# Kernel optimization log

Hardware: AMD Instinct MI355X
Metric: run time of the kernel (lower is better)

The kernel has to match this reference:

```python
import jax, jax.numpy as jnp
import numpy as np
from jax import lax

D_MODEL, D_INNER, D_STATE, D_CONV, DT_RANK = 128, 256, 16, 4, 8
BATCH, SEQ = 8, 4096


def setup_inputs() -> dict:
    key = jax.random.key(0)
    ks = jax.random.split(key, 13)
    g = lambda k, shape, fan: (jax.random.normal(k, shape, jnp.float32) / np.sqrt(fan)).astype(jnp.float32)
    inp = {
        "s": jax.random.normal(ks[0], (BATCH, SEQ, D_MODEL), jnp.float32),
        "in_proj_w": g(ks[1], (2 * D_INNER, D_MODEL), D_MODEL),
        "conv_w": g(ks[2], (D_INNER, 1, D_CONV), D_CONV),
        "conv_b": jnp.zeros((D_INNER,), jnp.float32),
        "x_proj_w": g(ks[3], (DT_RANK + 2 * D_STATE, D_INNER), D_INNER),
        "dt_proj_w": g(ks[4], (D_INNER, DT_RANK), DT_RANK),
        "dt_proj_b": jax.random.uniform(ks[5], (D_INNER,), jnp.float32, -4.0, -2.0),  # softplus(b) small, like mamba dt init
        "A_log": jnp.log(jnp.broadcast_to(jnp.arange(1, D_STATE + 1, dtype=jnp.float32), (D_INNER, D_STATE))),
        "D_skip": jnp.ones((D_INNER,), jnp.float32),
        "out_proj_w": g(ks[6], (D_MODEL, D_INNER), D_INNER),
        "ln_gamma": jnp.ones((D_MODEL,), jnp.float32),
        "ln_beta": jnp.zeros((D_MODEL,), jnp.float32),
        "fc_w": g(ks[7], (D_MODEL, D_MODEL), D_MODEL),
    }
    return inp


def _mamba(s, in_proj_w, conv_w, conv_b, x_proj_w, dt_proj_w, dt_proj_b, A_log, D_skip, out_proj_w):
    B, L, _ = s.shape
    xz = jnp.einsum("bld,ed->ble", s, in_proj_w)           # [B,L,2*D_INNER]
    x, z = jnp.split(xz, 2, axis=-1)                        # each [B,L,D_INNER]
    # causal depthwise conv1d
    xc = jnp.transpose(x, (0, 2, 1))                        # [B,D_INNER,L]
    xc = jnp.pad(xc, ((0, 0), (0, 0), (D_CONV - 1, 0)))
    xc = lax.conv_general_dilated(xc, conv_w, (1,), "VALID",
                                  dimension_numbers=("NCH", "OIH", "NCH"),
                                  feature_group_count=D_INNER)
    x = jax.nn.silu(jnp.transpose(xc + conv_b[None, :, None], (0, 2, 1)))  # [B,L,D_INNER]
    # input-dependent dt, B, C
    x_dbl = jnp.einsum("bld,ed->ble", x, x_proj_w)
    dt = x_dbl[..., :DT_RANK]
    Bc = x_dbl[..., DT_RANK:DT_RANK + D_STATE]              # [B,L,D_STATE]
    Cc = x_dbl[..., DT_RANK + D_STATE:]                     # [B,L,D_STATE]
    dt = jax.nn.softplus(jnp.einsum("blr,dr->bld", dt, dt_proj_w) + dt_proj_b)  # [B,L,D_INNER]
    A = -jnp.exp(A_log)                                     # [D_INNER,D_STATE]

    def step(h, inp):
        dt_t, b_t, c_t, u_t = inp                           # [B,Di],[B,Ds],[B,Ds],[B,Di]
        dA = jnp.exp(dt_t[:, :, None] * A)                  # [B,Di,Ds]
        dBu = (dt_t * u_t)[:, :, None] * b_t[:, None, :]
        h = dA * h + dBu
        y = jnp.einsum("bds,bs->bd", h, c_t)
        return h, y

    h0 = jnp.zeros((B, D_INNER, D_STATE), x.dtype)
    xs = (jnp.swapaxes(dt, 0, 1), jnp.swapaxes(Bc, 0, 1), jnp.swapaxes(Cc, 0, 1), jnp.swapaxes(x, 0, 1))
    _, ys = lax.scan(step, h0, xs)                          # ys: [L,B,D_INNER]
    y = jnp.swapaxes(ys, 0, 1) + x * D_skip
    y = y * jax.nn.silu(z)
    return jnp.einsum("bld,od->blo", y, out_proj_w)         # [B,L,D_MODEL]


def reference(s, in_proj_w, conv_w, conv_b, x_proj_w, dt_proj_w, dt_proj_b, A_log, D_skip, out_proj_w, ln_gamma, ln_beta, fc_w):
    h = _mamba(s, in_proj_w, conv_w, conv_b, x_proj_w, dt_proj_w, dt_proj_b, A_log, D_skip, out_proj_w)
    mu = jnp.mean(h, axis=-1, keepdims=True)
    var = jnp.mean(jnp.square(h - mu), axis=-1, keepdims=True)
    hn = (h - mu) * lax.rsqrt(var + 1e-5) * ln_gamma + ln_beta
    return jax.nn.relu(jnp.einsum("bld,od->blo", hn, fc_w))
```

## Files before the change

kernel.cpp:

```cpp
#include <hip/hip_runtime.h>
#include <math.h>

#define B_ 8
#define L_ 4096
#define DM 128
#define DI 256
#define DSN 16
#define RK 8
#define M_ (B_*L_)
#define NC 128
#define CH 32
#define CH2 64

typedef __attribute__((ext_vector_type(8))) short bfrag;
typedef __attribute__((ext_vector_type(4))) float ffrag;
typedef __attribute__((ext_vector_type(2))) float f32x2;

__device__ __forceinline__ float silu_f(float x) {
  return x * __builtin_amdgcn_rcpf(1.f + __expf(-x));
}
__device__ __forceinline__ float softplus_f(float x) {
  return (x > 20.f) ? x : __logf(1.f + __expf(x));
}

__device__ __forceinline__ unsigned short f2bf(float f) {
  unsigned int u = __builtin_bit_cast(unsigned int, f);
  unsigned int r = (u + 0x7FFFu + ((u >> 16) & 1u)) >> 16;
  return (unsigned short)r;
}
__device__ __forceinline__ unsigned int f2bf2(float lo, float hi) {
  return (unsigned int)f2bf(lo) | ((unsigned int)f2bf(hi) << 16);
}
__device__ __forceinline__ float bf2f(unsigned int us) {
  return __builtin_bit_cast(float, us << 16);
}

__global__ __launch_bounds__(256)
void gemm_bf16_in(const float* __restrict__ A, const float* __restrict__ W,
                  unsigned short* __restrict__ xb, unsigned short* __restrict__ zsb) {
  __shared__ unsigned short As[64 * 136];
  __shared__ unsigned short Ws[64 * 136];
  __shared__ unsigned short Os[64 * 72];
  const int t = threadIdx.x;
  const int m0 = blockIdx.y << 6;
  const int half = blockIdx.x;
  unsigned short* __restrict__ outp = half ? zsb : xb;
  const float* __restrict__ Wbase = W + (half << 8) * 128;
  for (int i = t; i < 64 * 32; i += 256) {
    int row = i >> 5, c4 = i & 31;
    float4 av = *(const float4*)&A[(m0 + row) * 128 + (c4 << 2)];
    uint2 ap = {f2bf2(av.x, av.y), f2bf2(av.z, av.w)};
    *(uint2*)&As[row * 136 + (c4 << 2)] = ap;
  }
  float4 wr[8];
#pragma unroll
  for (int k = 0; k < 8; ++k) {
    int i = t + (k << 8);
    int row = i >> 5, c4 = i & 31;
    wr[k] = *(const float4*)&Wbase[row * 128 + (c4 << 2)];
  }
#pragma unroll
  for (int k = 0; k < 8; ++k) {
    int i = t + (k << 8);
    int row = i >> 5, c4 = i & 31;
    uint2 wp = {f2bf2(wr[k].x, wr[k].y), f2bf2(wr[k].z, wr[k].w)};
    *(uint2*)&Ws[row * 136 + (c4 << 2)] = wp;
  }
  __syncthreads();
  const int w = t >> 6, l = t & 63, q = l >> 4, col = l & 15;
  for (int jt = 0; jt < 4; ++jt) {
    if (jt < 3) {
#pragma unroll
      for (int k = 0; k < 8; ++k) {
        int i = t + (k << 8);
        int row = i >> 5, c4 = i & 31;
        wr[k] = *(const float4*)&Wbase[(((jt + 1) << 6) + row) * 128 + (c4 << 2)];
      }
    }
    ffrag acc[4] = {{0.f,0.f,0.f,0.f},{0.f,0.f,0.f,0.f},{0.f,0.f,0.f,0.f},{0.f,0.f,0.f,0.f}};
#pragma unroll
    for (int s = 0; s < 4; ++s) {
      int k0 = s * 32 + q * 8;
      bfrag af = *(const bfrag*)&As[((w << 4) + col) * 136 + k0];
#pragma unroll
      for (int nt = 0; nt < 4; ++nt) {
        bfrag bf_ = *(const bfrag*)&Ws[((nt << 4) + col) * 136 + k0];
        acc[nt] = __builtin_amdgcn_mfma_f32_16x16x32_bf16(af, bf_, acc[nt], 0, 0, 0);
      }
    }
    __syncthreads();
#pragma unroll
    for (int nt = 0; nt < 4; ++nt)
#pragma unroll
      for (int i = 0; i < 4; ++i) {
        int ml = (w << 4) + (q << 2) + i;
        float v = acc[nt][i];
        if (half) v = silu_f(v);
        Os[ml * 72 + (nt << 4) + col] = f2bf(v);
      }
    if (jt < 3) {
#pragma unroll
      for (int k = 0; k < 8; ++k) {
        int i = t + (k << 8);
        int row = i >> 5, c4 = i & 31;
        uint2 wp = {f2bf2(wr[k].x, wr[k].y), f2bf2(wr[k].z, wr[k].w)};
        *(uint2*)&Ws[row * 136 + (c4 << 2)] = wp;
      }
    }
    __syncthreads();
    {
      int r = t >> 2, c8 = (t & 3) << 3;
      int m = m0 + r;
      *(uint4*)&outp[m * 256 + (jt << 6) + c8]      = *(const uint4*)&Os[r * 72 + c8];
      *(uint4*)&outp[m * 256 + (jt << 6) + 32 + c8] = *(const uint4*)&Os[r * 72 + 32 + c8];
    }
  }
}

__global__ __launch_bounds__(512)
void xproj_dtproj(const unsigned short* __restrict__ xb, const float* __restrict__ xw,
                  const float* __restrict__ dtw, const float* __restrict__ dtpb,
                  const float* __restrict__ cw, const float* __restrict__ cb,
                  const float* __restrict__ alog,
                  float* __restrict__ Bb, float* __restrict__ Cb,
                  unsigned int* __restrict__ udt,
                  unsigned short* __restrict__ cP, unsigned short* __restrict__ cHe) {
  __shared__ unsigned short ua[64 * 264];
  __shared__ unsigned short wb[48 * 264];
  __shared__ float dtr_s[64 * 12];
  __shared__ float Bs_l[64 * 16];
  const int t = threadIdx.x;
  const int p0 = blockIdx.x << 6;
  {
    const int k = t & 255, half = t >> 8;
    const int pstart = half << 5;
    const int base = p0 + pstart;
    const int lb = base & (L_ - 1);
    const float w0 = cw[k*4], w1 = cw[k*4+1], w2 = cw[k*4+2], w3 = cw[k*4+3];
    const float bias = cb[k];
    float x0 = (lb >= 3) ? bf2f((unsigned int)xb[(base - 3) * 256 + k]) : 0.f;
    float x1 = (lb >= 2) ? bf2f((unsigned int)xb[(base - 2) * 256 + k]) : 0.f;
    float x2 = (lb >= 1) ? bf2f((unsigned int)xb[(base - 1) * 256 + k]) : 0.f;
#pragma unroll 8
    for (int it = 0; it < 32; ++it) {
      float x3 = bf2f((unsigned int)xb[(base + it) * 256 + k]);
      float u = silu_f(fmaf(w0, x0, fmaf(w1, x1, fmaf(w2, x2, fmaf(w3, x3, bias)))));
      ua[(pstart + it) * 264 + k] = f2bf(u);
      x0 = x1; x1 = x2; x2 = x3;
    }
  }
  for (int i = t; i < 40 * 256; i += 512) {
    int n = i >> 8, k = i & 255;
    wb[n * 264 + k] = f2bf(xw[i]);
  }
  for (int i = t; i < 8 * 264; i += 512) wb[40 * 264 + i] = 0;
  __syncthreads();
  const int w = t >> 6, l = t & 63, q = l >> 4, col = l & 15;
  for (int tile = w; tile < 12; tile += 8) {
    const int mt = tile & 3, nt = tile >> 2;
    ffrag acc = {0.f, 0.f, 0.f, 0.f};
#pragma unroll
    for (int s = 0; s < 8; ++s) {
      int k0 = s * 32 + q * 8;
      bfrag af = *(const bfrag*)&ua[((mt << 4) + col) * 264 + k0];
      bfrag bf_ = *(const bfrag*)&wb[((nt << 4) + col) * 264 + k0];
      acc = __builtin_amdgcn_mfma_f32_16x16x32_bf16(af, bf_, acc, 0, 0, 0);
    }
#pragma unroll
    for (int i = 0; i < 4; ++i) {
      int ml = (mt << 4) + (q << 2) + i;
      int m = p0 + ml;
      if (nt == 0) {
        if (col < 8) dtr_s[ml * 12 + col] = acc[i];
        else {
          Bb[m * 16 + (col - 8)] = acc[i];
          Bs_l[ml * 16 + (col - 8)] = acc[i];
        }
      } else if (nt == 1) {
        if (col < 8) {
          Bb[m * 16 + 8 + col] = acc[i];
          Bs_l[ml * 16 + 8 + col] = acc[i];
        } else {
          Cb[m * 16 + (col - 8)] = acc[i];
        }
      } else {
        if (col < 8) Cb[m * 16 + 8 + col] = acc[i];
      }
    }
  }
  __syncthreads();
  {
    const int d = t & 255, half = t >> 8;
    const int pstart = half << 5;
    const int gpos = p0 + pstart;
    const int bb = gpos >> 12;
    const int cc = (gpos & (L_ - 1)) >> 5;
    const int bc = bb * NC + cc;
    float w8[8];
    *(float4*)&w8[0] = *(const float4*)&dtw[d * 8];
    *(float4*)&w8[4] = *(const float4*)&dtw[d * 8 + 4];
    const float bias = dtpb[d];
    float a[16];
    bool okl = true;
#pragma unroll
    for (int j = 0; j < 16; ++j) {
      a[j] = -__expf(alog[d * 16 + j]);
      float tgt = (float)(j + 1);
      okl = okl && (fabsf(a[j] + tgt) <= 1e-3f * tgt);
    }
    const bool fast = (bool)__all((int)okl);
    f32x2 h2[8] = {{0.f,0.f},{0.f,0.f},{0.f,0.f},{0.f,0.f},
                   {0.f,0.f},{0.f,0.f},{0.f,0.f},{0.f,0.f}};
    float sdt = 0.f;
#pragma unroll 2
    for (int pp = pstart; pp < pstart + 32; ++pp) {
      float r0[8];
      *(float4*)&r0[0] = *(const float4*)&dtr_s[pp * 12];
      *(float4*)&r0[4] = *(const float4*)&dtr_s[pp * 12 + 4];
      float a2 = bias;
#pragma unroll
      for (int r2 = 0; r2 < 8; ++r2) a2 = fmaf(r0[r2], w8[r2], a2);
      float sp = softplus_f(a2);
      unsigned int uq = (unsigned int)ua[pp * 264 + d];
      unsigned short spb = f2bf(sp);
      udt[(p0 + pp) * 256 + d] = uq | ((unsigned int)spb << 16);
      float dtv = bf2f((unsigned int)spb);
      float uv  = bf2f(uq);
      float du = dtv * uv;
      sdt += dtv;
      const float* brow = &Bs_l[pp * 16];
      float4 b0 = *(const float4*)&brow[0];
      float4 b1 = *(const float4*)&brow[4];
      float4 b2 = *(const float4*)&brow[8];
      float4 b3 = *(const float4*)&brow[12];
      f32x2 B2[8] = {{b0.x,b0.y},{b0.z,b0.w},{b1.x,b1.y},{b1.z,b1.w},
                     {b2.x,b2.y},{b2.z,b2.w},{b3.x,b3.y},{b3.z,b3.w}};
      f32x2 du2 = {du, du};
      if (fast) {
        float e1 = __expf(-dtv);
        float e2 = e1 * e1;
        f32x2 dA = {e1, e2};
        f32x2 e22 = {e2, e2};
#pragma unroll
        for (int jj = 0; jj < 8; ++jj) {
          h2[jj] = dA * h2[jj] + du2 * B2[jj];
          dA = dA * e22;
        }
      } else {
#pragma unroll
        for (int j = 0; j < 16; ++j) {
          float dA = __expf(dtv * a[j]);
          h2[j >> 1][j & 1] = fmaf(dA, h2[j >> 1][j & 1], du * B2[j >> 1][j & 1]);
        }
      }
    }
#pragma unroll
    for (int j = 0; j < 16; ++j) {
      int o = (bc * 16 + j) * 256 + d;
      cP[o]  = f2bf(__expf(a[j] * sdt));
      cHe[o] = f2bf(h2[j >> 1][j & 1]);
    }
  }
}

__global__ __launch_bounds__(512)
void scan_combine(unsigned short* __restrict__ cP, const unsigned short* __restrict__ cHe) {
  __shared__ float segP[64 * 9], segH[64 * 9], segS[64 * 9];
  const int t = threadIdx.x;
  const int sdl = t & 63, seg = t >> 6;
  const int blk = blockIdx.x;
  const int b = blk >> 6, grp = blk & 63;
  const int sd = (grp << 6) + sdl;
  const int base = b * NC * 4096 + sd;
  float Pacc = 1.f, Hacc = 0.f;
#pragma unroll
  for (int i = 0; i < 16; ++i) {
    int idx = base + (seg * 16 + i) * 4096;
    float p = bf2f((unsigned int)cP[idx]);
    float he = bf2f((unsigned int)cHe[idx]);
    Hacc = fmaf(p, Hacc, he);
    Pacc *= p;
  }
  segP[sdl * 9 + seg] = Pacc;
  segH[sdl * 9 + seg] = Hacc;
  __syncthreads();
  if (t < 64) {
    float hs = 0.f;
#pragma unroll
    for (int s2 = 0; s2 < 8; ++s2) {
      segS[t * 9 + s2] = hs;
      hs = fmaf(segP[t * 9 + s2], hs, segH[t * 9 + s2]);
    }
  }
  __syncthreads();
  float hs = segS[sdl * 9 + seg];
#pragma unroll
  for (int i = 0; i < 16; ++i) {
    int idx = base + (seg * 16 + i) * 4096;
    float p = bf2f((unsigned int)cP[idx]);
    float he = bf2f((unsigned int)cHe[idx]);
    cP[idx] = f2bf(hs);
    hs = fmaf(p, hs, he);
  }
}

__global__ __launch_bounds__(512, 4)
void scan3_out_ln_fc(const unsigned int* __restrict__ udt,
                     const float* __restrict__ Bb, const float* __restrict__ Cb,
                     const float* __restrict__ alog, const unsigned short* __restrict__ hst,
                     const float* __restrict__ dsk,
                     const unsigned short* __restrict__ zsb,
                     const float* __restrict__ W,
                     const float* __restrict__ gamma, const float* __restrict__ beta,
                     const float* __restrict__ fcw, float* __restrict__ out) {
  __shared__ float Bs[CH2 * 16];
  __shared__ float Cs[CH2 * 16];
  __shared__ unsigned short smA[64 * 264];
  __shared__ unsigned short smB[128 * 136];
  const int bc = blockIdx.x;
  const int b = bc >> 6, cc = bc & 63;
  const int t = threadIdx.x;
  const int l = t & 63, w = t >> 6;
  const int chh = t >> 8;
  const int d = t & 255;
  const int base = b * L_ + (cc << 1) * CH;
  const int cbase = base + chh * CH;
  const int hc = b * NC + (cc << 1) + chh;
  if (t < CH2 * 4)           ((float4*)Bs)[t]            = *(const float4*)&Bb[base * 16 + (t << 2)];
  else if (t < CH2 * 8)      ((float4*)Cs)[t - CH2 * 4]  = *(const float4*)&Cb[base * 16 + ((t - CH2 * 4) << 2)];
  float a[16];
  bool okl = true;
#pragma unroll
  for (int j = 0; j < 16; ++j) {
    a[j] = -__expf(alog[d * 16 + j]);
    float tgt = (float)(j + 1);
    okl = okl && (fabsf(a[j] + tgt) <= 1e-3f * tgt);
  }
  const bool fast = (bool)__all((int)okl);
  const float dskv = dsk[d];
  f32x2 h2[8];
#pragma unroll
  for (int jj = 0; jj < 8; ++jj) {
    h2[jj][0] = bf2f((unsigned int)hst[(hc * 16 + (jj << 1)) * 256 + d]);
    h2[jj][1] = bf2f((unsigned int)hst[(hc * 16 + (jj << 1) + 1) * 256 + d]);
  }
  unsigned int wv0 = udt[cbase * 256 + d];
  unsigned int wv1 = udt[(cbase + 1) * 256 + d];
  unsigned short zv0 = zsb[cbase * 256 + d];
  unsigned short zv1 = zsb[(cbase + 1) * 256 + d];
  __syncthreads();
#pragma unroll 2
  for (int ll = 0; ll < CH; ++ll) {
    const int l2 = (ll + 2 < CH) ? ll + 2 : CH - 1;
    unsigned int wv2 = udt[(cbase + l2) * 256 + d];
    unsigned short zv2 = zsb[(cbase + l2) * 256 + d];
    const float* brow = &Bs[(chh * CH + ll) * 16];
    const float* crow = &Cs[(chh * CH + ll) * 16];
    float4 b0 = *(const float4*)&brow[0];
    float4 b1 = *(const float4*)&brow[4];
    float4 b2 = *(const float4*)&brow[8];
    float4 b3 = *(const float4*)&brow[12];
    float4 c0 = *(const float4*)&crow[0];
    float4 c1 = *(const float4*)&crow[4];
    float4 c2 = *(const float4*)&crow[8];
    float4 c3 = *(const float4*)&crow[12];
    float uv  = bf2f(wv0 & 0xFFFFu);
    float dtv = bf2f(wv0 >> 16);
    f32x2 B2[8] = {{b0.x,b0.y},{b0.z,b0.w},{b1.x,b1.y},{b1.z,b1.w},
                   {b2.x,b2.y},{b2.z,b2.w},{b3.x,b3.y},{b3.z,b3.w}};
    f32x2 C2[8] = {{c0.x,c0.y},{c0.z,c0.w},{c1.x,c1.y},{c1.z,c1.w},
                   {c2.x,c2.y},{c2.z,c2.w},{c3.x,c3.y},{c3.z,c3.w}};
    float du = dtv * uv;
    f32x2 du2 = {du, du};
    f32x2 y2 = {0.f, 0.f};
    if (fast) {
      float e1 = __expf(-dtv);
      float e2 = e1 * e1;
      f32x2 dA = {e1, e2};
      f32x2 e22 = {e2, e2};
#pragma unroll
      for (int jj = 0; jj < 8; ++jj) {
        h2[jj] = dA * h2[jj] + du2 * B2[jj];
        y2 = y2 + h2[jj] * C2[jj];
        dA = dA * e22;
      }
    } else {
#pragma unroll
      for (int j = 0; j < 16; ++j) {
        float dA = __expf(dtv * a[j]);
        float hh = fmaf(dA, h2[j >> 1][j & 1], du * B2[j >> 1][j & 1]);
        h2[j >> 1][j & 1] = hh;
        y2[j & 1] = fmaf(hh, C2[j >> 1][j & 1], y2[j & 1]);
      }
    }
    float y = y2.x + y2.y;
    float zs = bf2f((unsigned int)zv0);
    smA[(chh * CH + ll) * 264 + d] = f2bf(fmaf(uv, dskv, y) * zs);
    wv0 = wv1; wv1 = wv2; zv0 = zv1; zv1 = zv2;
  }
  const int q = l >> 4, col = l & 15;
  ffrag acc[2][4];
  for (int nt2 = 0; nt2 < 2; ++nt2) {
    __syncthreads();
    for (int i = t; i < 64 * 64; i += 512) {
      int row = i >> 6, c4 = i & 63;
      float4 wv = *(const float4*)&W[((nt2 << 6) + row) * 256 + (c4 << 2)];
      uint2 wp = {f2bf2(wv.x, wv.y), f2bf2(wv.z, wv.w)};
      *(uint2*)&smB[row * 264 + (c4 << 2)] = wp;
    }
    __syncthreads();
    if (t < 256) {
#pragma unroll
      for (int nt = 0; nt < 4; ++nt) acc[nt2][nt] = (ffrag){0.f, 0.f, 0.f, 0.f};
#pragma unroll
      for (int s = 0; s < 8; ++s) {
        int k0 = s * 32 + q * 8;
        bfrag af = *(const bfrag*)&smA[((w << 4) + col) * 264 + k0];
#pragma unroll
        for (int nt = 0; nt < 4; ++nt) {
          bfrag bf_ = *(const bfrag*)&smB[((nt << 4) + col) * 264 + k0];
          acc[nt2][nt] = __builtin_amdgcn_mfma_f32_16x16x32_bf16(af, bf_, acc[nt2][nt], 0, 0, 0);
        }
      }
    }
  }
  float mu[4], rs[4];
  if (t < 256) {
#pragma unroll
    for (int i = 0; i < 4; ++i) {
      float s1 = 0.f, s2 = 0.f;
#pragma unroll
      for (int nt2 = 0; nt2 < 2; ++nt2)
#pragma unroll
        for (int nt = 0; nt < 4; ++nt) {
          float v = acc[nt2][nt][i];
          s1 += v; s2 = fmaf(v, v, s2);
        }
      s1 += __shfl_xor(s1, 1); s2 += __shfl_xor(s2, 1);
      s1 += __shfl_xor(s1, 2); s2 += __shfl_xor(s2, 2);
      s1 += __shfl_xor(s1, 4); s2 += __shfl_xor(s2, 4);
      s1 += __shfl_xor(s1, 8); s2 += __shfl_xor(s2, 8);
      mu[i] = s1 * (1.f / DM);
      float var = s2 * (1.f / DM) - mu[i] * mu[i];
      rs[i] = rsqrtf(var + 1e-5f);
    }
  }
  __syncthreads();
  if (t < 256) {
#pragma unroll
    for (int nt2 = 0; nt2 < 2; ++nt2)
#pragma unroll
      for (int nt = 0; nt < 4; ++nt) {
        int n = (nt2 << 6) + (nt << 4) + col;
        float g = gamma[n], be = beta[n];
#pragma unroll
        for (int i = 0; i < 4; ++i) {
          int r = (w << 4) + (q << 2) + i;
          smA[r * 136 + n] = f2bf(fmaf((acc[nt2][nt][i] - mu[i]) * rs[i], g, be));
        }
      }
  }
  for (int i = t; i < 128 * 32; i += 512) {
    int row = i >> 5, c4 = i & 31;
    float4 wv = *(const float4*)&fcw[row * 128 + (c4 << 2)];
    uint2 wp = {f2bf2(wv.x, wv.y), f2bf2(wv.z, wv.w)};
    *(uint2*)&smB[row * 136 + (c4 << 2)] = wp;
  }
  __syncthreads();
  if (t < 256) {
    ffrag a2[8] = {{0.f,0.f,0.f,0.f},{0.f,0.f,0.f,0.f},{0.f,0.f,0.f,0.f},{0.f,0.f,0.f,0.f},
                   {0.f,0.f,0.f,0.f},{0.f,0.f,0.f,0.f},{0.f,0.f,0.f,0.f},{0.f,0.f,0.f,0.f}};
#pragma unroll
    for (int s = 0; s < 4; ++s) {
      int k0 = s * 32 + q * 8;
      bfrag af = *(const bfrag*)&smA[((w << 4) + col) * 136 + k0];
#pragma unroll
      for (int nt = 0; nt < 8; ++nt) {
        bfrag bf_ = *(const bfrag*)&smB[((nt << 4) + col) * 136 + k0];
        a2[nt] = __builtin_amdgcn_mfma_f32_16x16x32_bf16(af, bf_, a2[nt], 0, 0, 0);
      }
    }
#pragma unroll
    for (int nt = 0; nt < 8; ++nt)
#pragma unroll
      for (int i = 0; i < 4; ++i) {
        int ml = (w << 4) + (q << 2) + i;
        out[(base + ml) * 128 + (nt << 4) + col] = fmaxf(a2[nt][i], 0.f);
      }
  }
}

extern "C" void kernel_launch(void* const* d_in, const int* in_sizes, int n_in,
                              void* d_out, int out_size, void* d_ws, size_t ws_size,
                              hipStream_t stream) {
  (void)in_sizes; (void)n_in; (void)out_size; (void)ws_size;
  const float* s    = (const float*)d_in[0];
  const float* w_in = (const float*)d_in[1];
  const float* cw   = (const float*)d_in[2];
  const float* cb   = (const float*)d_in[3];
  const float* xw   = (const float*)d_in[4];
  const float* dtw  = (const float*)d_in[5];
  const float* dtpb = (const float*)d_in[6];
  const float* alog = (const float*)d_in[7];
  const float* dsk  = (const float*)d_in[8];
  const float* ow   = (const float*)d_in[9];
  const float* gam  = (const float*)d_in[10];
  const float* bet  = (const float*)d_in[11];
  const float* fcw  = (const float*)d_in[12];
  float* out = (float*)d_out;
  float* ws  = (float*)d_ws;

  unsigned short* xb   = (unsigned short*)ws;
  unsigned short* zsb  = (unsigned short*)(ws + 4194304);
  unsigned int*   udt  = (unsigned int*)(ws + 8388608);
  float*          Bb   = ws + 16777216;
  float*          Cb   = ws + 17301504;
  unsigned short* cP   = (unsigned short*)(ws + 17825792);
  unsigned short* cHe  = (unsigned short*)(ws + 19922944);

  gemm_bf16_in<<<dim3(2, 512), 256, 0, stream>>>(s, w_in, xb, zsb);
  xproj_dtproj<<<512, 512, 0, stream>>>(xb, xw, dtw, dtpb, cw, cb, alog,
                                        Bb, Cb, udt, cP, cHe);
  scan_combine<<<512, 512, 0, stream>>>(cP, cHe);
  scan3_out_ln_fc<<<B_ * NC / 2, 512, 0, stream>>>(udt, Bb, Cb, alog, cP, dsk, zsb,
                                                   ow, gam, bet, fcw, out);
}
```

Baseline: 172.2 us.

## Fuse input projection GEMM into xproj kernel, keep x in shared memory

Removes the separate in_proj GEMM kernel and computes the x/z projection inside the xproj_dtproj block. x stays in shared memory, including a 16-row halo recomputed for the causal conv, so the bf16 xb tensor no longer makes a round trip through global memory and one launch is dropped. z is still computed here and written to global after SiLU. The cost is redundant halo rows, a larger shared pool (about 74KB) that may lower occupancy, and weight reloads done per 64-row block.

After: 168.7 us. -2.0%, faster.

```diff
diff --git a/kernel.cpp b/kernel.cpp
--- a/kernel.cpp
+++ b/kernel.cpp
@@ -35,102 +35,104 @@
   return __builtin_bit_cast(float, us << 16);
 }
 
-__global__ __launch_bounds__(256)
-void gemm_bf16_in(const float* __restrict__ A, const float* __restrict__ W,
-                  unsigned short* __restrict__ xb, unsigned short* __restrict__ zsb) {
-  __shared__ unsigned short As[64 * 136];
-  __shared__ unsigned short Ws[64 * 136];
-  __shared__ unsigned short Os[64 * 72];
-  const int t = threadIdx.x;
-  const int m0 = blockIdx.y << 6;
-  const int half = blockIdx.x;
-  unsigned short* __restrict__ outp = half ? zsb : xb;
-  const float* __restrict__ Wbase = W + (half << 8) * 128;
-  for (int i = t; i < 64 * 32; i += 256) {
-    int row = i >> 5, c4 = i & 31;
-    float4 av = *(const float4*)&A[(m0 + row) * 128 + (c4 << 2)];
-    uint2 ap = {f2bf2(av.x, av.y), f2bf2(av.z, av.w)};
-    *(uint2*)&As[row * 136 + (c4 << 2)] = ap;
-  }
-  float4 wr[8];
-#pragma unroll
-  for (int k = 0; k < 8; ++k) {
-    int i = t + (k << 8);
-    int row = i >> 5, c4 = i & 31;
-    wr[k] = *(const float4*)&Wbase[row * 128 + (c4 << 2)];
-  }
-#pragma unroll
-  for (int k = 0; k < 8; ++k) {
-    int i = t + (k << 8);
-    int row = i >> 5, c4 = i & 31;
-    uint2 wp = {f2bf2(wr[k].x, wr[k].y), f2bf2(wr[k].z, wr[k].w)};
-    *(uint2*)&Ws[row * 136 + (c4 << 2)] = wp;
-  }
-  __syncthreads();
-  const int w = t >> 6, l = t & 63, q = l >> 4, col = l & 15;
-  for (int jt = 0; jt < 4; ++jt) {
-    if (jt < 3) {
-#pragma unroll
-      for (int k = 0; k < 8; ++k) {
-        int i = t + (k << 8);
-        int row = i >> 5, c4 = i & 31;
-        wr[k] = *(const float4*)&Wbase[(((jt + 1) << 6) + row) * 128 + (c4 << 2)];
-      }
-    }
-    ffrag acc[4] = {{0.f,0.f,0.f,0.f},{0.f,0.f,0.f,0.f},{0.f,0.f,0.f,0.f},{0.f,0.f,0.f,0.f}};
-#pragma unroll
-    for (int s = 0; s < 4; ++s) {
-      int k0 = s * 32 + q * 8;
-      bfrag af = *(const bfrag*)&As[((w << 4) + col) * 136 + k0];
-#pragma unroll
-      for (int nt = 0; nt < 4; ++nt) {
-        bfrag bf_ = *(const bfrag*)&Ws[((nt << 4) + col) * 136 + k0];
-        acc[nt] = __builtin_amdgcn_mfma_f32_16x16x32_bf16(af, bf_, acc[nt], 0, 0, 0);
-      }
-    }
-    __syncthreads();
-#pragma unroll
-    for (int nt = 0; nt < 4; ++nt)
-#pragma unroll
-      for (int i = 0; i < 4; ++i) {
-        int ml = (w << 4) + (q << 2) + i;
-        float v = acc[nt][i];
-        if (half) v = silu_f(v);
-        Os[ml * 72 + (nt << 4) + col] = f2bf(v);
-      }
-    if (jt < 3) {
-#pragma unroll
-      for (int k = 0; k < 8; ++k) {
-        int i = t + (k << 8);
-        int row = i >> 5, c4 = i & 31;
-        uint2 wp = {f2bf2(wr[k].x, wr[k].y), f2bf2(wr[k].z, wr[k].w)};
-        *(uint2*)&Ws[row * 136 + (c4 << 2)] = wp;
-      }
-    }
-    __syncthreads();
-    {
-      int r = t >> 2, c8 = (t & 3) << 3;
-      int m = m0 + r;
-      *(uint4*)&outp[m * 256 + (jt << 6) + c8]      = *(const uint4*)&Os[r * 72 + c8];
-      *(uint4*)&outp[m * 256 + (jt << 6) + 32 + c8] = *(const uint4*)&Os[r * 72 + 32 + c8];
-    }
-  }
-}
-
-__global__ __launch_bounds__(512)
-void xproj_dtproj(const unsigned short* __restrict__ xb, const float* __restrict__ xw,
+__global__ __launch_bounds__(512, 4)
+void xproj_dtproj(const float* __restrict__ s, const float* __restrict__ w_in,
+                  const float* __restrict__ xw,
                   const float* __restrict__ dtw, const float* __restrict__ dtpb,
                   const float* __restrict__ cw, const float* __restrict__ cb,
                   const float* __restrict__ alog,
                   float* __restrict__ Bb, float* __restrict__ Cb,
                   unsigned int* __restrict__ udt,
+                  unsigned short* __restrict__ zsb,
                   unsigned short* __restrict__ cP, unsigned short* __restrict__ cHe) {
-  __shared__ unsigned short ua[64 * 264];
-  __shared__ unsigned short wb[48 * 264];
-  __shared__ float dtr_s[64 * 12];
-  __shared__ float Bs_l[64 * 16];
+  __shared__ __align__(16) char pool[74544];
+  unsigned short* As = (unsigned short*)pool;
+  unsigned short* Ws = (unsigned short*)(pool + 21760);
+  unsigned short* ua = (unsigned short*)pool;
+  unsigned short* hx = (unsigned short*)(pool + 39168);
+  unsigned short* wb = (unsigned short*)(pool + 39168);
+  float* dtr_s = (float*)(pool + 64512);
+  float* Bs_l  = (float*)(pool + 67584);
   const int t = threadIdx.x;
   const int p0 = blockIdx.x << 6;
+  const int w = t >> 6, l = t & 63, q = l >> 4, col = l & 15;
+
+  for (int i = t; i < 80 * 32; i += 512) {
+    int row = i >> 5, c4 = i & 31;
+    int pos = (row < 64) ? (p0 + row) : (p0 - 16 + (row - 64));
+    if (pos < 0) pos = 0;
+    float4 av = *(const float4*)&s[pos * 128 + (c4 << 2)];
+    uint2 ap = {f2bf2(av.x, av.y), f2bf2(av.z, av.w)};
+    *(uint2*)&As[row * 136 + (c4 << 2)] = ap;
+  }
+  float4 wr[4];
+#pragma unroll
+  for (int k = 0; k < 4; ++k) {
+    int i = t + (k << 9);
+    int row = i >> 5, c4 = i & 31;
+    wr[k] = *(const float4*)&w_in[row * 128 + (c4 << 2)];
+  }
+#pragma unroll
+  for (int k = 0; k < 4; ++k) {
+    int i = t + (k << 9);
+    int row = i >> 5, c4 = i & 31;
+    uint2 wp = {f2bf2(wr[k].x, wr[k].y), f2bf2(wr[k].z, wr[k].w)};
+    *(uint2*)&Ws[row * 136 + (c4 << 2)] = wp;
+  }
+  __syncthreads();
+  for (int jt = 0; jt < 8; ++jt) {
+    if (jt < 7) {
+#pragma unroll
+      for (int k = 0; k < 4; ++k) {
+        int i = t + (k << 9);
+        int row = i >> 5, c4 = i & 31;
+        wr[k] = *(const float4*)&w_in[(((jt + 1) << 6) + row) * 128 + (c4 << 2)];
+      }
+    }
+    const int T = (jt < 4) ? 20 : 16;
+    for (int tile = w; tile < T; tile += 8) {
+      const int mt = tile >> 2, nt = tile & 3;
+      ffrag acc = {0.f, 0.f, 0.f, 0.f};
+#pragma unroll
+      for (int s8 = 0; s8 < 4; ++s8) {
+        int k0 = s8 * 32 + q * 8;
+        bfrag af = *(const bfrag*)&As[((mt << 4) + col) * 136 + k0];
+        bfrag bf_ = *(const bfrag*)&Ws[((nt << 4) + col) * 136 + k0];
+        acc = __builtin_amdgcn_mfma_f32_16x16x32_bf16(af, bf_, acc, 0, 0, 0);
+      }
+      if (jt < 4) {
+        const int ch = (jt << 6) + (nt << 4) + col;
+#pragma unroll
+        for (int i = 0; i < 4; ++i) {
+          int rt = (q << 2) + i;
+          if (mt < 4) {
+            hx[(3 + (mt << 4) + rt) * 264 + ch] = f2bf(acc[i]);
+          } else {
+            int hr = rt - 13;
+            if (hr >= 0) hx[hr * 264 + ch] = f2bf(acc[i]);
+          }
+        }
+      } else {
+        const int ch = ((jt - 4) << 6) + (nt << 4) + col;
+#pragma unroll
+        for (int i = 0; i < 4; ++i) {
+          int m = p0 + (mt << 4) + (q << 2) + i;
+          zsb[m * 256 + ch] = f2bf(silu_f(acc[i]));
+        }
+      }
+    }
+    __syncthreads();
+    if (jt < 7) {
+#pragma unroll
+      for (int k = 0; k < 4; ++k) {
+        int i = t + (k << 9);
+        int row = i >> 5, c4 = i & 31;
+        uint2 wp = {f2bf2(wr[k].x, wr[k].y), f2bf2(wr[k].z, wr[k].w)};
+        *(uint2*)&Ws[row * 136 + (c4 << 2)] = wp;
+      }
+      __syncthreads();
+    }
+  }
   {
     const int k = t & 255, half = t >> 8;
     const int pstart = half << 5;
@@ -138,30 +140,30 @@
     const int lb = base & (L_ - 1);
     const float w0 = cw[k*4], w1 = cw[k*4+1], w2 = cw[k*4+2], w3 = cw[k*4+3];
     const float bias = cb[k];
-    float x0 = (lb >= 3) ? bf2f((unsigned int)xb[(base - 3) * 256 + k]) : 0.f;
-    float x1 = (lb >= 2) ? bf2f((unsigned int)xb[(base - 2) * 256 + k]) : 0.f;
-    float x2 = (lb >= 1) ? bf2f((unsigned int)xb[(base - 1) * 256 + k]) : 0.f;
+    float x0 = (lb >= 3) ? bf2f((unsigned int)hx[(pstart + 0) * 264 + k]) : 0.f;
+    float x1 = (lb >= 2) ? bf2f((unsigned int)hx[(pstart + 1) * 264 + k]) : 0.f;
+    float x2 = (lb >= 1) ? bf2f((unsigned int)hx[(pstart + 2) * 264 + k]) : 0.f;
 #pragma unroll 8
     for (int it = 0; it < 32; ++it) {
-      float x3 = bf2f((unsigned int)xb[(base + it) * 256 + k]);
+      float x3 = bf2f((unsigned int)hx[(pstart + 3 + it) * 264 + k]);
       float u = silu_f(fmaf(w0, x0, fmaf(w1, x1, fmaf(w2, x2, fmaf(w3, x3, bias)))));
       ua[(pstart + it) * 264 + k] = f2bf(u);
       x0 = x1; x1 = x2; x2 = x3;
     }
   }
+  __syncthreads();
   for (int i = t; i < 40 * 256; i += 512) {
     int n = i >> 8, k = i & 255;
     wb[n * 264 + k] = f2bf(xw[i]);
   }
   for (int i = t; i < 8 * 264; i += 512) wb[40 * 264 + i] = 0;
   __syncthreads();
-  const int w = t >> 6, l = t & 63, q = l >> 4, col = l & 15;
   for (int tile = w; tile < 12; tile += 8) {
     const int mt = tile & 3, nt = tile >> 2;
     ffrag acc = {0.f, 0.f, 0.f, 0.f};
 #pragma unroll
-    for (int s = 0; s < 8; ++s) {
-      int k0 = s * 32 + q * 8;
+    for (int s8 = 0; s8 < 8; ++s8) {
+      int k0 = s8 * 32 + q * 8;
       bfrag af = *(const bfrag*)&ua[((mt << 4) + col) * 264 + k0];
       bfrag bf_ = *(const bfrag*)&wb[((nt << 4) + col) * 264 + k0];
       acc = __builtin_amdgcn_mfma_f32_16x16x32_bf16(af, bf_, acc, 0, 0, 0);
@@ -413,8 +415,8 @@
 #pragma unroll
       for (int nt = 0; nt < 4; ++nt) acc[nt2][nt] = (ffrag){0.f, 0.f, 0.f, 0.f};
 #pragma unroll
-      for (int s = 0; s < 8; ++s) {
-        int k0 = s * 32 + q * 8;
+      for (int s8 = 0; s8 < 8; ++s8) {
+        int k0 = s8 * 32 + q * 8;
         bfrag af = *(const bfrag*)&smA[((w << 4) + col) * 264 + k0];
 #pragma unroll
         for (int nt = 0; nt < 4; ++nt) {
@@ -471,8 +473,8 @@
     ffrag a2[8] = {{0.f,0.f,0.f,0.f},{0.f,0.f,0.f,0.f},{0.f,0.f,0.f,0.f},{0.f,0.f,0.f,0.f},
                    {0.f,0.f,0.f,0.f},{0.f,0.f,0.f,0.f},{0.f,0.f,0.f,0.f},{0.f,0.f,0.f,0.f}};
 #pragma unroll
-    for (int s = 0; s < 4; ++s) {
-      int k0 = s * 32 + q * 8;
+    for (int s8 = 0; s8 < 4; ++s8) {
+      int k0 = s8 * 32 + q * 8;
       bfrag af = *(const bfrag*)&smA[((w << 4) + col) * 136 + k0];
 #pragma unroll
       for (int nt = 0; nt < 8; ++nt) {
@@ -510,7 +512,6 @@
   float* out = (float*)d_out;
   float* ws  = (float*)d_ws;
 
-  unsigned short* xb   = (unsigned short*)ws;
   unsigned short* zsb  = (unsigned short*)(ws + 4194304);
   unsigned int*   udt  = (unsigned int*)(ws + 8388608);
   float*          Bb   = ws + 16777216;
@@ -518,9 +519,8 @@
   unsigned short* cP   = (unsigned short*)(ws + 17825792);
   unsigned short* cHe  = (unsigned short*)(ws + 19922944);
 
-  gemm_bf16_in<<<dim3(2, 512), 256, 0, stream>>>(s, w_in, xb, zsb);
-  xproj_dtproj<<<512, 512, 0, stream>>>(xb, xw, dtw, dtpb, cw, cb, alog,
-                                        Bb, Cb, udt, cP, cHe);
+  xproj_dtproj<<<512, 512, 0, stream>>>(s, w_in, xw, dtw, dtpb, cw, cb, alog,
+                                        Bb, Cb, udt, zsb, cP, cHe);
   scan_combine<<<512, 512, 0, stream>>>(cP, cHe);
   scan3_out_ln_fc<<<B_ * NC / 2, 512, 0, stream>>>(udt, Bb, Cb, alog, cP, dsk, zsb,
                                                    ow, gam, bet, fcw, out);
```
